# Performance work log

Hardware: AMD Instinct MI355X
Metric: run time of the kernel (lower is better)

Reference implementation:

```python
import jax, jax.numpy as jnp
import numpy as np

L, H, D = 4, 8, 256  # layers, heads, feature dim (Z has d+1 = 257 channels)
B, N1 = 8, 2048      # batch, N+1 tokens (N = 2047 context + 1 query)
STD = 0.02


def setup_inputs() -> dict:
    key = jax.random.key(0)
    k1, k2 = jax.random.split(key)
    Z = jax.random.normal(k1, (B, N1, D + 1), dtype=jnp.float32)
    allparam = STD * jax.random.normal(k2, (L, H, 2, D, D), dtype=jnp.float32)
    return {"Z": Z, "allparam": allparam}


def _attention(P, Q, Z):
    # P, Q: (d, d); Z: (B, N+1, d+1). act is None -> purely bilinear.
    Bn, N1_, d1 = Z.shape
    N, d = N1_ - 1, d1 - 1
    # Zero-padded (d+1, d+1) versions: P_full has a 1 in the label corner.
    P_full = jnp.zeros((d + 1, d + 1), Z.dtype).at[:d, :d].set(P).at[d, d].set(1.0)
    Q_full = jnp.zeros((d + 1, d + 1), Z.dtype).at[:d, :d].set(Q)
    sim = jnp.einsum('BNi,ij,BMj->BNM', Z, Q_full, Z)   # (B, N+1, N+1)
    val = jnp.einsum('ij,BNj->BNi', P_full, Z)            # (B, N+1, d+1)
    # A = eye(N+1) with A[N, N] = 0  ->  sim @ A @ val == sim @ (val with last token zeroed)
    val = val.at[:, N, :].set(0.0)
    return jnp.einsum('BNM,BMi->BNi', sim, val) / N


def reference(Z, allparam):
    for i in range(L):
        res = 0.0
        for j in range(H):  # small fixed head loop, matches torch structure
            P = allparam[i, j, 0]
            Q = allparam[i, j, 1]
            res = res + _attention(P, Q, Z)
        Z = Z + res
    return Z
```

## Files before the change

### kernel.cpp

```cpp
#include <hip/hip_runtime.h>


#define NL   4
#define NH   8
#define DD   256
#define NCH  257
#define NTOK 2048
#define NVAL 2047
#define NB   8

typedef short  short8v __attribute__((ext_vector_type(8)));
typedef short  short4v __attribute__((ext_vector_type(4)));
typedef float  f32x4   __attribute__((ext_vector_type(4)));

__device__ __forceinline__ unsigned short f2b(float x) {
  union { float f; unsigned u; } v; v.f = x;
  unsigned u = v.u + 0x7fffu + ((v.u >> 16) & 1u);
  return (unsigned short)(u >> 16);
}
__device__ __forceinline__ float b2f(short s) {
  union { unsigned u; float f; } v; v.u = ((unsigned)(unsigned short)s) << 16;
  return v.f;
}

__device__ __forceinline__ void mm64(const short* A, const short* B, int lda, int ldb,
                                     int ar, int bc, int k0, int k1, int lane,
                                     f32x4 (&acc)[4][4]) {
  #pragma unroll 2
  for (int kk = k0; kk < k1; kk += 32) {
    const int kc = kk + ((lane >> 4) << 3);
    short8v av[4], bv[4];
    #pragma unroll
    for (int f = 0; f < 4; ++f)
      av[f] = *(const short8v*)(A + (size_t)(ar + f * 16 + (lane & 15)) * lda + kc);
    #pragma unroll
    for (int g = 0; g < 4; ++g)
      bv[g] = *(const short8v*)(B + (size_t)(bc + g * 16 + (lane & 15)) * ldb + kc);
    #pragma unroll
    for (int f = 0; f < 4; ++f)
      #pragma unroll
      for (int g = 0; g < 4; ++g)
        acc[f][g] = __builtin_amdgcn_mfma_f32_16x16x32_bf16(av[f], bv[g], acc[f][g], 0, 0, 0);
  }
}

__global__ __launch_bounds__(256) void k_init(const float* __restrict__ Zin,
                                              const float* __restrict__ ap,
                                              short* __restrict__ Pbf, short* __restrict__ Qcat2,
                                              float* __restrict__ QsumT,
                                              short* __restrict__ Zxbf, short* __restrict__ Zxt,
                                              float* __restrict__ zlab, float* __restrict__ zlabtrue) {
  __shared__ float lds[64][65];
  const int bx = blockIdx.x, tid = threadIdx.x;
  if (bx < 1024) {
    const f32x4* src = (const f32x4*)ap;
    int q0 = (bx * 256 + tid) * 2;
    #pragma unroll
    for (int u = 0; u < 2; ++u) {
      int q = q0 + u, lj = q >> 14, rc4 = q & 16383;
      f32x4 v = src[(size_t)(lj * 2) * 16384 + rc4];
      short4v o;
      #pragma unroll
      for (int i = 0; i < 4; ++i) o[i] = (short)f2b(v[i]);
      ((short4v*)Pbf)[(size_t)lj * 16384 + rc4] = o;
    }
    return;
  }
  if (bx < 2048) {
    int idx = bx - 1024;
    int l = idx >> 8, k = idx & 255;
    int j = tid >> 5, t0 = (tid & 31) * 8;
    const float* s = ap + (size_t)((l * 8 + j) * 2 + 1) * 65536 + (size_t)k * 256 + t0;
    f32x4 a = *(const f32x4*)s, bq = *(const f32x4*)(s + 4);
    short8v o;
    #pragma unroll
    for (int i = 0; i < 4; ++i) { o[i] = (short)f2b(a[i]); o[4 + i] = (short)f2b(bq[i]); }
    *(short8v*)(Qcat2 + (size_t)(l * 256 + k) * 2048 + j * 256 + t0) = o;
    return;
  }
  if (bx < 2112) {
    int qb = bx - 2048;
    int l = qb >> 4, xx = qb & 15;
    int k0 = (xx >> 2) * 64, t0 = (xx & 3) * 64;
    int c = tid & 63, r = tid >> 6;
    #pragma unroll
    for (int i = 0; i < 16; ++i) {
      int k = r + i * 4;
      float s = 0.f;
      #pragma unroll
      for (int j = 0; j < 8; ++j)
        s += ap[(size_t)((l * 8 + j) * 2 + 1) * 65536 + (size_t)(k0 + k) * 256 + (t0 + c)];
      lds[k][c] = s;
    }
    __syncthreads();
    #pragma unroll
    for (int i = 0; i < 16; ++i) {
      int tl = r + i * 4;
      QsumT[(size_t)l * 65536 + (size_t)(t0 + tl) * 256 + (k0 + c)] = lds[c][tl];
    }
    return;
  }
  int tb = bx - 2112;
  int x = tb & 3, y = (tb >> 2) & 31, b = tb >> 7;
  int k0 = x * 64, m0 = y * 64;
  int c = tid & 63, r = tid >> 6;
  #pragma unroll
  for (int i = 0; i < 16; ++i) {
    int mrow = r + i * 4, m = m0 + mrow;
    float v = Zin[((size_t)b * NTOK + m) * NCH + k0 + c];
    lds[mrow][c] = v;
    Zxbf[((size_t)b * NTOK + m) * DD + k0 + c] = (short)f2b(v);
  }
  if (x == 0 && tid < 64) {
    int m = m0 + tid;
    float lv = Zin[((size_t)b * NTOK + m) * NCH + DD];
    zlabtrue[b * NTOK + m] = lv;
    zlab[b * NTOK + m] = (m == NVAL) ? 0.f : lv;
  }
  __syncthreads();
  const int mt = tid & 15, kg = tid >> 4;
  #pragma unroll
  for (int i = 0; i < 4; ++i) {
    int krow = kg * 4 + i;
    int m4 = mt * 4;
    short4v o;
    #pragma unroll
    for (int q = 0; q < 4; ++q) {
      float v = lds[m4 + q][krow];
      o[q] = (m0 + m4 + q == NVAL) ? (short)0 : (short)f2b(v);
    }
    *(short4v*)(Zxt + ((size_t)b * DD + k0 + krow) * NTOK + m0 + m4) = o;
  }
}

__global__ __launch_bounds__(256) void k_gram(const short* __restrict__ Zxt,
                                              const short* __restrict__ Zxbf,
                                              const float* __restrict__ zlab,
                                              short* __restrict__ Gacc,
                                              float* __restrict__ gcolacc) {
  __shared__ float zl[256];
  const int x = blockIdx.x, tid = threadIdx.x;
  if (x >= 512) {
    const int idx = x - 512, b = idx & 7, seg = idx >> 3;
    zl[tid] = zlab[b * NTOK + seg * 256 + tid];
    __syncthreads();
    const short* base = Zxbf + ((size_t)b * NTOK + seg * 256) * DD + tid;
    float s = 0.f;
    #pragma unroll 8
    for (int m = 0; m < 256; ++m) s += b2f(base[(size_t)m * DD]) * zl[m];
    gcolacc[(seg * 8 + b) * 256 + tid] = s;
    return;
  }
  const int lane = tid & 63, wid = tid >> 6;
  const int b = x & 7, t = (x >> 3) & 3, seg = x >> 5;
  const int r0 = (t >> 1) * 128, c0 = (t & 1) * 128;
  const int ar = r0 + (wid >> 1) * 64, bc = c0 + (wid & 1) * 64;
  const short* A = Zxt + (size_t)b * DD * NTOK;
  f32x4 acc[4][4];
  #pragma unroll
  for (int f = 0; f < 4; ++f) for (int g = 0; g < 4; ++g) for (int i = 0; i < 4; ++i) acc[f][g][i] = 0.f;
  mm64(A, A, NTOK, NTOK, ar, bc, seg * 128, seg * 128 + 128, lane, acc);
  short* out = Gacc + (size_t)(seg * 8 + b) * 65536;
  #pragma unroll
  for (int f = 0; f < 4; ++f) {
    const int rb = ar + f * 16 + ((lane >> 4) << 2);
    #pragma unroll
    for (int g = 0; g < 4; ++g) {
      const int col = bc + g * 16 + (lane & 15);
      short4v p;
      #pragma unroll
      for (int i = 0; i < 4; ++i) p[i] = (short)f2b(acc[f][g][i]);
      *(short4v*)(out + (size_t)col * 256 + rb) = p;
    }
  }
}

__global__ __launch_bounds__(256) void k_gred(const short* __restrict__ Gacc,
                                              const float* __restrict__ gcolacc,
                                              short* __restrict__ Gbf, float* __restrict__ gcol) {
  const int x = blockIdx.x, tid = threadIdx.x;
  if (x >= 256) {
    const int b = x - 256;
    float s = 0.f;
    #pragma unroll
    for (int seg = 0; seg < 8; ++seg) s += gcolacc[(seg * 8 + b) * 256 + tid];
    gcol[b * 256 + tid] = s;
    return;
  }
  const int b = x & 7, chunk = x >> 3;
  const int i0 = chunk * 2048 + tid * 8;
  float s[8] = {};
  #pragma unroll
  for (int seg = 0; seg < 16; ++seg) {
    short8v v = *(const short8v*)(Gacc + (size_t)(seg * 8 + b) * 65536 + i0);
    #pragma unroll
    for (int q = 0; q < 8; ++q) s[q] += b2f(v[q]);
  }
  short8v o;
  #pragma unroll
  for (int q = 0; q < 8; ++q) o[q] = (short)f2b(s[q]);
  *(short8v*)(Gbf + (size_t)b * 65536 + i0) = o;
}

__global__ __launch_bounds__(256) void k_pv(const short* __restrict__ Gbf, const short* __restrict__ Pbf,
                                            const float* __restrict__ QsumT, const float* __restrict__ gcol,
                                            short* __restrict__ Vt3, float* __restrict__ mcol, int layer) {
  __shared__ float gs[256];
  const int x = blockIdx.x, tid = threadIdx.x;
  if (x >= 256) {
    const int b = x - 256;
    gs[tid] = gcol[b * 256 + tid];
    __syncthreads();
    float s = 0.f;
    for (int t = 0; t < 256; ++t) s += QsumT[(size_t)layer * 65536 + (size_t)t * 256 + tid] * gs[t];
    mcol[b * 256 + tid] = s * (1.0f / (float)NVAL);
    return;
  }
  const int lane = tid & 63, wid = tid >> 6;
  const int b = x & 7, t = x >> 3;
  const int r0 = (t & 1) * 128, c0 = (t >> 1) * 128;
  const int ar = r0 + (wid >> 1) * 64, bc = c0 + (wid & 1) * 64;
  const short* A = Gbf + (size_t)b * 65536;
  const short* B = Pbf + (size_t)layer * 8 * 65536;
  f32x4 acc[4][4];
  #pragma unroll
  for (int f = 0; f < 4; ++f) for (int g = 0; g < 4; ++g) for (int i = 0; i < 4; ++i) acc[f][g][i] = 0.f;
  mm64(A, B, 256, 256, ar, bc, 0, 256, lane, acc);
  short* out = Vt3 + (size_t)b * 524288;
  #pragma unroll
  for (int f = 0; f < 4; ++f) {
    const int tt0 = ar + f * 16 + ((lane >> 4) << 2);
    #pragma unroll
    for (int g = 0; g < 4; ++g) {
      const int jc = bc + g * 16 + (lane & 15);
      const int j = jc >> 8, c = jc & 255;
      short4v p;
      #pragma unroll
      for (int i = 0; i < 4; ++i) p[i] = (short)f2b(acc[f][g][i]);
      *(short4v*)(out + (size_t)c * 2048 + j * 256 + tt0) = p;
    }
  }
}

__global__ __launch_bounds__(256) void k_qm(const short* __restrict__ Vt3, const short* __restrict__ Qcat2,
                                            short* __restrict__ Macc, int layer) {
  const int x = blockIdx.x, tid = threadIdx.x;
  const int lane = tid & 63, wid = tid >> 6;
  const int b = x & 7, t = (x >> 3) & 3, seg = x >> 5;
  const int r0 = (t >> 1) * 128, c0 = (t & 1) * 128;
  const int ar = r0 + (wid >> 1) * 64, bc = c0 + (wid & 1) * 64;
  const short* A = Qcat2 + (size_t)layer * 524288;
  const short* B = Vt3 + (size_t)b * 524288;
  f32x4 acc[4][4];
  #pragma unroll
  for (int f = 0; f < 4; ++f) for (int g = 0; g < 4; ++g) for (int i = 0; i < 4; ++i) acc[f][g][i] = 0.f;
  mm64(A, B, 2048, 2048, ar, bc, seg * 128, seg * 128 + 128, lane, acc);
  short* out = Macc + (size_t)(seg * 8 + b) * 65536;
  #pragma unroll
  for (int f = 0; f < 4; ++f) {
    const int kb = ar + f * 16 + ((lane >> 4) << 2);
    #pragma unroll
    for (int g = 0; g < 4; ++g) {
      const int c = bc + g * 16 + (lane & 15);
      short4v p;
      #pragma unroll
      for (int i = 0; i < 4; ++i) p[i] = (short)f2b(acc[f][g][i]);
      *(short4v*)(out + (size_t)c * 256 + kb) = p;
    }
  }
}

__global__ __launch_bounds__(256) void k_mred(const short* __restrict__ Macc, short* __restrict__ Mt) {
  const int x = blockIdx.x, tid = threadIdx.x;
  const int b = x & 7, chunk = x >> 3;
  const int i0 = chunk * 2048 + tid * 8;
  float s[8] = {};
  #pragma unroll
  for (int seg = 0; seg < 16; ++seg) {
    short8v v = *(const short8v*)(Macc + (size_t)(seg * 8 + b) * 65536 + i0);
    #pragma unroll
    for (int q = 0; q < 8; ++q) s[q] += b2f(v[q]);
  }
  const float invN = 1.0f / (float)NVAL;
  short8v o;
  #pragma unroll
  for (int q = 0; q < 8; ++q) o[q] = (short)f2b(s[q] * invN);
  *(short8v*)(Mt + (size_t)b * 65536 + i0) = o;
}

__global__ __launch_bounds__(256) void k_apply(const short* __restrict__ Zxin, const short* __restrict__ Mt,
                                               const float* __restrict__ mcol,
                                               short* __restrict__ Zxout, short* __restrict__ Zxt_out,
                                               float* __restrict__ zlab, float* __restrict__ zlabtrue,
                                               float* __restrict__ dout, int wnext) {
  __shared__ short ldsT[128][136];
  const int tid = threadIdx.x, lane = tid & 63, wid = tid >> 6;
  const int wr = wid >> 1, wc = wid & 1;
  const int x = blockIdx.x;
  const int b = x & 7, t = x >> 3;
  const int ar_wg = (t >> 1) * 128, bc_wg = (t & 1) * 128;
  const int ar = ar_wg + wr * 64, bc = bc_wg + wc * 64;
  const short* A = Zxin + (size_t)b * NTOK * DD;
  const short* B = Mt + (size_t)b * 65536;
  const bool gemv = ((t & 1) == 0 && wc == 0);
  f32x4 acc[4][4];
  #pragma unroll
  for (int f = 0; f < 4; ++f) for (int g = 0; g < 4; ++g) for (int i = 0; i < 4; ++i) acc[f][g][i] = 0.f;
  float s[4] = {0.f, 0.f, 0.f, 0.f};
  #pragma unroll 2
  for (int kk = 0; kk < 256; kk += 32) {
    const int kc = kk + ((lane >> 4) << 3);
    short8v av[4], bv[4];
    #pragma unroll
    for (int f = 0; f < 4; ++f)
      av[f] = *(const short8v*)(A + (size_t)(ar + f * 16 + (lane & 15)) * DD + kc);
    #pragma unroll
    for (int g = 0; g < 4; ++g)
      bv[g] = *(const short8v*)(B + (size_t)(bc + g * 16 + (lane & 15)) * 256 + kc);
    if (gemv) {
      const float* mp = mcol + b * 256 + kc;
      f32x4 m0 = *(const f32x4*)mp, m1 = *(const f32x4*)(mp + 4);
      #pragma unroll
      for (int f = 0; f < 4; ++f) {
        #pragma unroll
        for (int q = 0; q < 4; ++q) {
          s[f] += b2f(av[f][q]) * m0[q];
          s[f] += b2f(av[f][4 + q]) * m1[q];
        }
      }
    }
    #pragma unroll
    for (int f = 0; f < 4; ++f)
      #pragma unroll
      for (int g = 0; g < 4; ++g)
        acc[f][g] = __builtin_amdgcn_mfma_f32_16x16x32_bf16(av[f], bv[g], acc[f][g], 0, 0, 0);
  }
  #pragma unroll
  for (int f = 0; f < 4; ++f) {
    const int nb = ar + f * 16 + ((lane >> 4) << 2);
    #pragma unroll
    for (int g = 0; g < 4; ++g) {
      const int c = bc + g * 16 + (lane & 15);
      #pragma unroll
      for (int i = 0; i < 4; ++i) {
        const size_t ridx = ((size_t)b * NTOK + nb + i) * DD + c;
        float nv = b2f(Zxin[ridx]) + acc[f][g][i];
        if (wnext) {
          unsigned short bvv = f2b(nv);
          Zxout[ridx] = (short)bvv;
          ldsT[c - bc_wg][nb - ar_wg + i] = (nb + i == NVAL) ? (short)0 : (short)bvv;
        } else {
          dout[((size_t)b * NTOK + nb + i) * NCH + c] = nv;
        }
      }
    }
  }
  if (gemv) {
    #pragma unroll
    for (int f = 0; f < 4; ++f) {
      float tt = s[f];
      tt += __shfl_xor(tt, 16);
      tt += __shfl_xor(tt, 32);
      if ((lane >> 4) == 0) {
        int n = ar + f * 16 + (lane & 15);
        float nv = zlabtrue[b * NTOK + n] + tt;
        if (wnext) {
          zlabtrue[b * NTOK + n] = nv;
          zlab[b * NTOK + n] = (n == NVAL) ? 0.f : nv;
        } else {
          dout[((size_t)b * NTOK + n) * NCH + DD] = nv;
        }
      }
    }
  }
  if (wnext) {
    __syncthreads();
    const int n0 = (tid & 15) * 8, cr0 = (tid >> 4) * 8;
    #pragma unroll
    for (int r = 0; r < 8; ++r) {
      short8v v = *(const short8v*)&ldsT[cr0 + r][n0];
      *(short8v*)(Zxt_out + ((size_t)b * DD + bc_wg + cr0 + r) * NTOK + ar_wg + n0) = v;
    }
  }
}

extern "C" void kernel_launch(void* const* d_in, const int* in_sizes, int n_in,
                              void* d_out, int out_size, void* d_ws, size_t ws_size,
                              hipStream_t stream) {
  const float* Zin      = (const float*)d_in[0];
  const float* allparam = (const float*)d_in[1];
  float* Z = (float*)d_out;

  const size_t o_zx0  = 0;
  const size_t o_zx1  = o_zx0  + 8388608;
  const size_t o_zxt  = o_zx1  + 8388608;
  const size_t o_acc  = o_zxt  + 8388608;
  const size_t o_gbf  = o_acc  + 16777216;
  const size_t o_vt   = o_gbf  + 1048576;
  const size_t o_mt   = o_vt   + 8388608;
  const size_t o_pbf  = o_mt   + 1048576;
  const size_t o_qc2  = o_pbf  + 4194304;
  const size_t o_qsum = o_qc2  + 4194304;
  const size_t o_gca  = o_qsum + 1048576;
  const size_t o_gcol = o_gca  + 65536;
  const size_t o_mcol = o_gcol + 8192;
  const size_t o_zlab = o_mcol + 8192;
  const size_t o_zlt  = o_zlab + 65536;
  const size_t NEED   = o_zlt  + 65536;
  if (ws_size < NEED) return;

  char* wsb = (char*)d_ws;
  short* Zx[2]   = { (short*)(wsb + o_zx0), (short*)(wsb + o_zx1) };
  short* Zxt     = (short*)(wsb + o_zxt);
  short* Acc     = (short*)(wsb + o_acc);
  short* Gbf     = (short*)(wsb + o_gbf);
  short* Vt3     = (short*)(wsb + o_vt);
  short* Mt      = (short*)(wsb + o_mt);
  short* Pbf     = (short*)(wsb + o_pbf);
  short* Qcat2   = (short*)(wsb + o_qc2);
  float* QsumT   = (float*)(wsb + o_qsum);
  float* gcolacc = (float*)(wsb + o_gca);
  float* gcol    = (float*)(wsb + o_gcol);
  float* mcol    = (float*)(wsb + o_mcol);
  float* zlab    = (float*)(wsb + o_zlab);
  float* zlabtrue= (float*)(wsb + o_zlt);

  k_init<<<dim3(3136), dim3(256), 0, stream>>>(Zin, allparam, Pbf, Qcat2, QsumT,
                                               Zx[0], Zxt, zlab, zlabtrue);

  for (int layer = 0; layer < NL; ++layer) {
    const int cur = layer & 1;
    const int wnext = (layer < NL - 1) ? 1 : 0;
    k_gram<<<dim3(576), dim3(256), 0, stream>>>(Zxt, Zx[cur], zlab, Acc, gcolacc);
    k_gred<<<dim3(264), dim3(256), 0, stream>>>(Acc, gcolacc, Gbf, gcol);
    k_pv<<<dim3(264), dim3(256), 0, stream>>>(Gbf, Pbf, QsumT, gcol, Vt3, mcol, layer);
    k_qm<<<dim3(512), dim3(256), 0, stream>>>(Vt3, Qcat2, Acc, layer);
    k_mred<<<dim3(256), dim3(256), 0, stream>>>(Acc, Mt);
    k_apply<<<dim3(256), dim3(256), 0, stream>>>(Zx[cur], Mt, mcol,
                                                 Zx[cur ^ 1], Zxt, zlab, zlabtrue,
                                                 Z, wnext);
  }
}
```

Baseline: 358.5 us.

## Exploit Gram symmetry and shrink per-block tiles in pv and apply kernels

The Gram kernel now computes only three of the four 128x128 quadrants of the symmetric Z^T Z matrix. The off-diagonal block writes both its output and its transpose, which cuts the MFMA work and the block count. The k_pv and k_apply kernels drop from 128x128 to 64x128 tiles per workgroup, doubling the grid to improve occupancy and CU coverage on the 256-CU device. The costs are uncoalesced scalar transpose stores in the Gram kernel and more reloading of A tiles across blocks.

```diff
diff --git a/kernel.cpp b/kernel.cpp
--- a/kernel.cpp
+++ b/kernel.cpp
@@ -23,23 +23,24 @@
   return v.f;
 }
 
-__device__ __forceinline__ void mm64(const short* A, const short* B, int lda, int ldb,
+template <int NF, int NG>
+__device__ __forceinline__ void mm_t(const short* A, const short* B, int lda, int ldb,
                                      int ar, int bc, int k0, int k1, int lane,
-                                     f32x4 (&acc)[4][4]) {
+                                     f32x4 (&acc)[NF][NG]) {
   #pragma unroll 2
   for (int kk = k0; kk < k1; kk += 32) {
     const int kc = kk + ((lane >> 4) << 3);
-    short8v av[4], bv[4];
-    #pragma unroll
-    for (int f = 0; f < 4; ++f)
+    short8v av[NF], bv[NG];
+    #pragma unroll
+    for (int f = 0; f < NF; ++f)
       av[f] = *(const short8v*)(A + (size_t)(ar + f * 16 + (lane & 15)) * lda + kc);
     #pragma unroll
-    for (int g = 0; g < 4; ++g)
+    for (int g = 0; g < NG; ++g)
       bv[g] = *(const short8v*)(B + (size_t)(bc + g * 16 + (lane & 15)) * ldb + kc);
     #pragma unroll
-    for (int f = 0; f < 4; ++f)
-      #pragma unroll
-      for (int g = 0; g < 4; ++g)
+    for (int f = 0; f < NF; ++f)
+      #pragma unroll
+      for (int g = 0; g < NG; ++g)
         acc[f][g] = __builtin_amdgcn_mfma_f32_16x16x32_bf16(av[f], bv[g], acc[f][g], 0, 0, 0);
   }
 }
@@ -140,8 +141,8 @@
                                               float* __restrict__ gcolacc) {
   __shared__ float zl[256];
   const int x = blockIdx.x, tid = threadIdx.x;
-  if (x >= 512) {
-    const int idx = x - 512, b = idx & 7, seg = idx >> 3;
+  if (x >= 384) {
+    const int idx = x - 384, b = idx & 7, seg = idx >> 3;
     zl[tid] = zlab[b * NTOK + seg * 256 + tid];
     __syncthreads();
     const short* base = Zxbf + ((size_t)b * NTOK + seg * 256) * DD + tid;
@@ -152,14 +153,16 @@
     return;
   }
   const int lane = tid & 63, wid = tid >> 6;
-  const int b = x & 7, t = (x >> 3) & 3, seg = x >> 5;
-  const int r0 = (t >> 1) * 128, c0 = (t & 1) * 128;
+  const int b = x & 7, r = x >> 3;
+  const int q = r % 3, seg = r / 3;
+  const int r0 = (q == 1) ? 128 : 0;
+  const int c0 = (q == 0) ? 0 : 128;
   const int ar = r0 + (wid >> 1) * 64, bc = c0 + (wid & 1) * 64;
   const short* A = Zxt + (size_t)b * DD * NTOK;
   f32x4 acc[4][4];
   #pragma unroll
   for (int f = 0; f < 4; ++f) for (int g = 0; g < 4; ++g) for (int i = 0; i < 4; ++i) acc[f][g][i] = 0.f;
-  mm64(A, A, NTOK, NTOK, ar, bc, seg * 128, seg * 128 + 128, lane, acc);
+  mm_t<4, 4>(A, A, NTOK, NTOK, ar, bc, seg * 128, seg * 128 + 128, lane, acc);
   short* out = Gacc + (size_t)(seg * 8 + b) * 65536;
   #pragma unroll
   for (int f = 0; f < 4; ++f) {
@@ -171,6 +174,11 @@
       #pragma unroll
       for (int i = 0; i < 4; ++i) p[i] = (short)f2b(acc[f][g][i]);
       *(short4v*)(out + (size_t)col * 256 + rb) = p;
+      if (q == 2) {
+        #pragma unroll
+        for (int i = 0; i < 4; ++i)
+          out[(size_t)(rb + i) * 256 + col] = p[i];
+      }
     }
   }
 }
@@ -207,8 +215,8 @@
                                             short* __restrict__ Vt3, float* __restrict__ mcol, int layer) {
   __shared__ float gs[256];
   const int x = blockIdx.x, tid = threadIdx.x;
-  if (x >= 256) {
-    const int b = x - 256;
+  if (x >= 512) {
+    const int b = x - 512;
     gs[tid] = gcol[b * 256 + tid];
     __syncthreads();
     float s = 0.f;
@@ -218,20 +226,20 @@
   }
   const int lane = tid & 63, wid = tid >> 6;
   const int b = x & 7, t = x >> 3;
-  const int r0 = (t & 1) * 128, c0 = (t >> 1) * 128;
-  const int ar = r0 + (wid >> 1) * 64, bc = c0 + (wid & 1) * 64;
+  const int r0 = (t & 3) * 64, jc0 = (t >> 2) * 128;
+  const int bc = jc0 + wid * 32;
   const short* A = Gbf + (size_t)b * 65536;
   const short* B = Pbf + (size_t)layer * 8 * 65536;
-  f32x4 acc[4][4];
-  #pragma unroll
-  for (int f = 0; f < 4; ++f) for (int g = 0; g < 4; ++g) for (int i = 0; i < 4; ++i) acc[f][g][i] = 0.f;
-  mm64(A, B, 256, 256, ar, bc, 0, 256, lane, acc);
+  f32x4 acc[4][2];
+  #pragma unroll
+  for (int f = 0; f < 4; ++f) for (int g = 0; g < 2; ++g) for (int i = 0; i < 4; ++i) acc[f][g][i] = 0.f;
+  mm_t<4, 2>(A, B, 256, 256, r0, bc, 0, 256, lane, acc);
   short* out = Vt3 + (size_t)b * 524288;
   #pragma unroll
   for (int f = 0; f < 4; ++f) {
-    const int tt0 = ar + f * 16 + ((lane >> 4) << 2);
-    #pragma unroll
-    for (int g = 0; g < 4; ++g) {
+    const int tt0 = r0 + f * 16 + ((lane >> 4) << 2);
+    #pragma unroll
+    for (int g = 0; g < 2; ++g) {
       const int jc = bc + g * 16 + (lane & 15);
       const int j = jc >> 8, c = jc & 255;
       short4v p;
@@ -254,7 +262,7 @@
   f32x4 acc[4][4];
   #pragma unroll
   for (int f = 0; f < 4; ++f) for (int g = 0; g < 4; ++g) for (int i = 0; i < 4; ++i) acc[f][g][i] = 0.f;
-  mm64(A, B, 2048, 2048, ar, bc, seg * 128, seg * 128 + 128, lane, acc);
+  mm_t<4, 4>(A, B, 2048, 2048, ar, bc, seg * 128, seg * 128 + 128, lane, acc);
   short* out = Macc + (size_t)(seg * 8 + b) * 65536;
   #pragma unroll
   for (int f = 0; f < 4; ++f) {
@@ -293,29 +301,28 @@
                                                short* __restrict__ Zxout, short* __restrict__ Zxt_out,
                                                float* __restrict__ zlab, float* __restrict__ zlabtrue,
                                                float* __restrict__ dout, int wnext) {
-  __shared__ short ldsT[128][136];
+  __shared__ short ldsT[128][72];
   const int tid = threadIdx.x, lane = tid & 63, wid = tid >> 6;
-  const int wr = wid >> 1, wc = wid & 1;
   const int x = blockIdx.x;
   const int b = x & 7, t = x >> 3;
-  const int ar_wg = (t >> 1) * 128, bc_wg = (t & 1) * 128;
-  const int ar = ar_wg + wr * 64, bc = bc_wg + wc * 64;
+  const int n0 = (t >> 1) * 64, c0 = (t & 1) * 128;
+  const int bc = c0 + wid * 32;
   const short* A = Zxin + (size_t)b * NTOK * DD;
   const short* B = Mt + (size_t)b * 65536;
-  const bool gemv = ((t & 1) == 0 && wc == 0);
-  f32x4 acc[4][4];
-  #pragma unroll
-  for (int f = 0; f < 4; ++f) for (int g = 0; g < 4; ++g) for (int i = 0; i < 4; ++i) acc[f][g][i] = 0.f;
+  const bool gemv = ((t & 1) == 0 && wid == 0);
+  f32x4 acc[4][2];
+  #pragma unroll
+  for (int f = 0; f < 4; ++f) for (int g = 0; g < 2; ++g) for (int i = 0; i < 4; ++i) acc[f][g][i] = 0.f;
   float s[4] = {0.f, 0.f, 0.f, 0.f};
   #pragma unroll 2
   for (int kk = 0; kk < 256; kk += 32) {
     const int kc = kk + ((lane >> 4) << 3);
-    short8v av[4], bv[4];
+    short8v av[4], bv[2];
     #pragma unroll
     for (int f = 0; f < 4; ++f)
-      av[f] = *(const short8v*)(A + (size_t)(ar + f * 16 + (lane & 15)) * DD + kc);
-    #pragma unroll
-    for (int g = 0; g < 4; ++g)
+      av[f] = *(const short8v*)(A + (size_t)(n0 + f * 16 + (lane & 15)) * DD + kc);
+    #pragma unroll
+    for (int g = 0; g < 2; ++g)
       bv[g] = *(const short8v*)(B + (size_t)(bc + g * 16 + (lane & 15)) * 256 + kc);
     if (gemv) {
       const float* mp = mcol + b * 256 + kc;
@@ -332,14 +339,14 @@
     #pragma unroll
     for (int f = 0; f < 4; ++f)
       #pragma unroll
-      for (int g = 0; g < 4; ++g)
+      for (int g = 0; g < 2; ++g)
         acc[f][g] = __builtin_amdgcn_mfma_f32_16x16x32_bf16(av[f], bv[g], acc[f][g], 0, 0, 0);
   }
   #pragma unroll
   for (int f = 0; f < 4; ++f) {
-    const int nb = ar + f * 16 + ((lane >> 4) << 2);
-    #pragma unroll
-    for (int g = 0; g < 4; ++g) {
+    const int nb = n0 + f * 16 + ((lane >> 4) << 2);
+    #pragma unroll
+    for (int g = 0; g < 2; ++g) {
       const int c = bc + g * 16 + (lane & 15);
       #pragma unroll
       for (int i = 0; i < 4; ++i) {
@@ -348,7 +355,7 @@
         if (wnext) {
           unsigned short bvv = f2b(nv);
           Zxout[ridx] = (short)bvv;
-          ldsT[c - bc_wg][nb - ar_wg + i] = (nb + i == NVAL) ? (short)0 : (short)bvv;
+          ldsT[c - c0][nb - n0 + i] = (nb + i == NVAL) ? (short)0 : (short)bvv;
         } else {
           dout[((size_t)b * NTOK + nb + i) * NCH + c] = nv;
         }
@@ -362,7 +369,7 @@
       tt += __shfl_xor(tt, 16);
       tt += __shfl_xor(tt, 32);
       if ((lane >> 4) == 0) {
-        int n = ar + f * 16 + (lane & 15);
+        int n = n0 + f * 16 + (lane & 15);
         float nv = zlabtrue[b * NTOK + n] + tt;
         if (wnext) {
           zlabtrue[b * NTOK + n] = nv;
@@ -375,11 +382,12 @@
   }
   if (wnext) {
     __syncthreads();
-    const int n0 = (tid & 15) * 8, cr0 = (tid >> 4) * 8;
-    #pragma unroll
-    for (int r = 0; r < 8; ++r) {
-      short8v v = *(const short8v*)&ldsT[cr0 + r][n0];
-      *(short8v*)(Zxt_out + ((size_t)b * DD + bc_wg + cr0 + r) * NTOK + ar_wg + n0) = v;
+    #pragma unroll
+    for (int u = 0; u < 4; ++u) {
+      const int e = tid + u * 256;
+      const int cr = e >> 3, ch = e & 7;
+      short8v v = *(const short8v*)&ldsT[cr][ch * 8];
+      *(short8v*)(Zxt_out + ((size_t)b * DD + c0 + cr) * NTOK + n0 + ch * 8) = v;
     }
   }
 }
@@ -431,12 +439,12 @@
   for (int layer = 0; layer < NL; ++layer) {
     const int cur = layer & 1;
     const int wnext = (layer < NL - 1) ? 1 : 0;
-    k_gram<<<dim3(576), dim3(256), 0, stream>>>(Zxt, Zx[cur], zlab, Acc, gcolacc);
+    k_gram<<<dim3(448), dim3(256), 0, stream>>>(Zxt, Zx[cur], zlab, Acc, gcolacc);
     k_gred<<<dim3(264), dim3(256), 0, stream>>>(Acc, gcolacc, Gbf, gcol);
-    k_pv<<<dim3(264), dim3(256), 0, stream>>>(Gbf, Pbf, QsumT, gcol, Vt3, mcol, layer);
+    k_pv<<<dim3(520), dim3(256), 0, stream>>>(Gbf, Pbf, QsumT, gcol, Vt3, mcol, layer);
     k_qm<<<dim3(512), dim3(256), 0, stream>>>(Vt3, Qcat2, Acc, layer);
     k_mred<<<dim3(256), dim3(256), 0, stream>>>(Acc, Mt);
-    k_apply<<<dim3(256), dim3(256), 0, stream>>>(Zx[cur], Mt, mcol,
+    k_apply<<<dim3(512), dim3(256), 0, stream>>>(Zx[cur], Mt, mcol,
                                                  Zx[cur ^ 1], Zxt, zlab, zlabtrue,
                                                  Z, wnext);
   }
```

Measured after the change: 354.3 us. Within noise of the previous version (-1.2%).
